# Kernel optimization log

Measured on AMD Instinct MI355X. Metric: run time of the kernel, lower is better.

Reference implementation:

```python
import jax, jax.numpy as jnp
import numpy as np

B, H, E, V = 128, 1024, 1024, 40000
L, S, A = 256, 10, 10
L_S, L_A = 1.0, 1.0  # s_copy_lambda / a_copy_lambda
NEG = -1e24


def setup_inputs():
    key = jax.random.key(0)
    ks = jax.random.split(key, 32)
    n = lambda i, shape: jax.random.normal(ks[i], shape, dtype=jnp.float32)
    p = lambda i, shape: jax.random.normal(ks[i], shape, dtype=jnp.float32) * 0.02
    rnn_in = 3 * E + H  # embed + history ctx (H) + state ctx (E) + action ctx (E)
    return {
        "inp": n(0, (B, 1, E)),
        "hidden": n(1, (1, B, H)),
        "hs_vectors": n(2, (B, L, H)),
        "state_gumbel_prob": jax.random.uniform(ks[3], (B, S, V), dtype=jnp.float32),
        "state_gumbel_embed": n(4, (B, S, E)),
        "action_gumbel_prob": jax.random.uniform(ks[5], (B, A, V), dtype=jnp.float32),
        "action_gumbel_embed": n(6, (B, A, E)),
        "history_lens": jax.random.randint(ks[7], (B,), 1, L + 1),
        "history_word_indices": jax.random.randint(ks[8], (B, L), 0, V),
        # history word mlp-attention
        "Wq_hist": p(9, (H, H)), "bq_hist": jnp.zeros((H,), jnp.float32),
        "Wm_hist": p(10, (H, H)), "v_hist": p(11, (H,)),
        # init_s_attn / init_a_attn (query H, memory E)
        "Wq_s": p(12, (H, H)), "bq_s": jnp.zeros((H,), jnp.float32),
        "Wm_s": p(13, (E, H)), "v_s": p(14, (H,)),
        "Wq_a": p(15, (H, H)), "bq_a": jnp.zeros((H,), jnp.float32),
        "Wm_a": p(16, (E, H)), "v_a": p(17, (H,)),
        # sparse_copy_attn (memory E+1)
        "Wq_sc": p(18, (H, H)), "bq_sc": jnp.zeros((H,), jnp.float32),
        "Wm_sc": p(19, (E + 1, H)), "v_sc": p(20, (H,)),
        # GRU (torch layout: [3H, in], gate order r,z,n)
        "W_ih": p(21, (3 * H, rnn_in)), "W_hh": p(22, (3 * H, H)),
        "b_ih": jnp.zeros((3 * H,), jnp.float32), "b_hh": jnp.zeros((3 * H,), jnp.float32),
        # output projection
        "W_out": p(23, (H, V)), "b_out": jnp.zeros((V,), jnp.float32),
    }


def _mlp_scores(q, mem, Wq, bq, Wm, v):
    # q: [B,1,H], mem: [B,L,M] -> additive-attention logits [B,1,L]
    t = jnp.tanh((q @ Wq + bq) + (mem @ Wm))  # [B,L,H]
    return (t @ v)[:, None, :]


def reference(inp, hidden, hs_vectors, state_gumbel_prob, state_gumbel_embed,
              action_gumbel_prob, action_gumbel_embed, history_lens,
              history_word_indices, Wq_hist, bq_hist, Wm_hist, v_hist,
              Wq_s, bq_s, Wm_s, v_s, Wq_a, bq_a, Wm_a, v_a,
              Wq_sc, bq_sc, Wm_sc, v_sc, W_ih, W_hh, b_ih, b_hh, W_out, b_out):
    q0 = jnp.transpose(hidden, (1, 0, 2))  # [B,1,H]
    # --- history word attention (masked mlp attention) ---
    hist_scores = _mlp_scores(q0, hs_vectors, Wq_hist, bq_hist, Wm_hist, v_hist)
    valid = jnp.arange(L)[None, None, :] < history_lens[:, None, None]
    hist_scores = jnp.where(valid, hist_scores, NEG)
    c_his = jax.nn.softmax(hist_scores, axis=-1) @ hs_vectors  # [B,1,H]
    # --- init_consult over state / action gumbel embeddings ---
    sw = jax.nn.softmax(_mlp_scores(q0, state_gumbel_embed, Wq_s, bq_s, Wm_s, v_s), axis=-1)
    c_state = sw @ state_gumbel_embed  # [B,1,E]
    aw = jax.nn.softmax(_mlp_scores(q0, action_gumbel_embed, Wq_a, bq_a, Wm_a, v_a), axis=-1)
    c_action = aw @ action_gumbel_embed  # [B,1,E]
    x = jnp.concatenate([inp, c_his, c_state, c_action], axis=-1)[:, 0, :]  # [B,3E+H]
    # --- single-step GRU cell (torch semantics, gate order r,z,n) ---
    h0 = hidden[0]
    gi = x @ W_ih.T + b_ih
    gh = h0 @ W_hh.T + b_hh
    ir, iz, inn = jnp.split(gi, 3, axis=-1)
    hr, hz, hn = jnp.split(gh, 3, axis=-1)
    r = jax.nn.sigmoid(ir + hr)
    z = jax.nn.sigmoid(iz + hz)
    nact = jnp.tanh(inn + r * hn)
    h_new = (1.0 - z) * nact + z * h0  # [B,H]
    # --- vocab logits + copy logits, joint softmax ---
    gene_logits = h_new @ W_out + b_out  # [B,V]
    cq = h_new[:, None, :]
    hs_logits = jnp.einsum('bqh,blh->bql', cq, hs_vectors)[:, 0, :]  # dot attn, [B,L]
    s_tag = jnp.zeros((B, S, 1), jnp.float32)
    a_tag = jnp.ones((B, A, 1), jnp.float32)
    st_logits = _mlp_scores(cq, jnp.concatenate([state_gumbel_embed, s_tag], -1), Wq_sc, bq_sc, Wm_sc, v_sc)[:, 0, :]
    ac_logits = _mlp_scores(cq, jnp.concatenate([action_gumbel_embed, a_tag], -1), Wq_sc, bq_sc, Wm_sc, v_sc)[:, 0, :]
    all_logits = jnp.concatenate([gene_logits, hs_logits, st_logits, ac_logits], axis=-1)
    wp = jax.nn.softmax(all_logits, axis=-1)  # [B, V+L+S+A]
    gene_p = wp[:, :V]
    hs_w = wp[:, V:V + L]
    st_w = wp[:, V + L:V + L + S]
    ac_w = wp[:, V + L + S:]
    # --- copy-distribution mixing ---
    scp = jnp.einsum('bs,bsv->bv', st_w, state_gumbel_prob)
    acp = jnp.einsum('ba,bav->bv', ac_w, action_gumbel_prob)
    gene_p = gene_p + L_S * scp + L_A * acp
    copy_p = jnp.zeros((B, V), jnp.float32).at[jnp.arange(B)[:, None], history_word_indices].add(hs_w)
    out = jnp.log(gene_p + copy_p)[:, None, :]  # [B,1,V]
    return out, h_new[None]
```

## Files before the change

kernel.cpp:

```cpp
#include <hip/hip_runtime.h>
#include <stdint.h>

typedef __attribute__((ext_vector_type(4))) float f32x4;
typedef __attribute__((ext_vector_type(2))) unsigned int u32x2;
typedef __attribute__((ext_vector_type(4))) unsigned int u32x4;
typedef __attribute__((ext_vector_type(8))) short bf16x8;

#define BV (128*40000)

__device__ __forceinline__ unsigned rne_bf16(float f) {
    unsigned x = __float_as_uint(f);
    return ((x + 0x7FFFu + ((x >> 16) & 1u)) >> 16) & 0xFFFFu;
}
__device__ __forceinline__ unsigned pack2(float a, float b) {
    return rne_bf16(a) | (rne_bf16(b) << 16);
}
__device__ __forceinline__ float bf2f(unsigned u) {
    return __uint_as_float((u & 0xFFFFu) << 16);
}
__device__ __forceinline__ float sigm(float x) { return 1.0f / (1.0f + expf(-x)); }
__device__ __forceinline__ float ftanh(float x) {
    float e = __expf(2.0f * x);
    return 1.0f - 2.0f / (e + 1.0f);
}

__device__ __forceinline__ void gload16(const void* g, void* l) {
    __builtin_amdgcn_global_load_lds(
        (const __attribute__((address_space(1))) unsigned*)g,
        (__attribute__((address_space(3))) unsigned*)l, 16, 0, 0);
}

struct BigArgs {
    const unsigned short *hs, *WmhT, *se, *ae, *WmsT, *WmaT, *WmscT;
    const float *qh_h, *bq_h, *v_h;
    const float *qh_s, *bq_s, *v_s;
    const float *qh_a, *bq_a, *v_a;
    float *hsc, *stsc, *acsc;
    unsigned short *mseh, *maeh;
};

__global__ __launch_bounds__(512, 1) void k_big(
    BigArgs a, int* __restrict__ ctr, const int* __restrict__ prefix,
    const int* __restrict__ ntp) {
    __shared__ unsigned short As[2][16384];
    __shared__ unsigned short Bs[2][16384];
    __shared__ int sTile;
    __shared__ int rows_tab[256];

    const int nTiles = ntp[0], Mp = ntp[1];
    const int t = threadIdx.x, lane = t & 63, wv = t >> 6;
    const int l16 = lane & 15, lq = lane >> 4;
    const int wm = wv >> 2, wn = wv & 3;
    const int srowL = t >> 3;
    const int gccA = ((t & 7) ^ (srowL & 7)) << 3;
    const int swz = l16 & 7;
    const int c0 = ((lq ^ swz) << 3);
    const int A0 = (wm << 13) + (l16 << 6);
    const int B0 = ((wn >> 1) << 13) + ((((wn & 1) << 6) + l16) << 6);

#define STQA(ktt, d, q) gload16(gAr[q] + (ktt) * 64, &As[d][((q) << 12) + (wv << 9)])
#define STQB(ktt, d, q) gload16(gB + ((size_t)(q) << 16) + (ktt) * 64, &Bs[d][((q) << 12) + (wv << 9)])

    for (;;) {
        __syncthreads();
        if (t == 0) sTile = atomicAdd(ctr, 1);
        __syncthreads();
        const int wg = sTile;
        if (wg >= nTiles) return;

        const unsigned short *Abase, *Bt;
        const float *rb = nullptr, *cb = nullptr, *vv = nullptr;
        float* out = nullptr;
        unsigned short* outh = nullptr;
        int m0, n0, vrows, cls;
        if (wg < 40) {
            cls = 0;
            int op = wg / 20, r = wg - op * 20;
            int mt = r >> 2, nt2 = r & 3;
            if (op == 0) { Abase = a.se; Bt = a.WmsT; rb = a.qh_s; cb = a.bq_s; vv = a.v_s; out = a.stsc; }
            else         { Abase = a.ae; Bt = a.WmaT; rb = a.qh_a; cb = a.bq_a; vv = a.v_a; out = a.acsc; }
            m0 = mt << 8; n0 = nt2 << 8; vrows = 256;
        } else if (wg < 80) {
            cls = 1;
            int r = wg - 40;
            int op = r / 20; r -= op * 20;
            int mt = r >> 2, nt2 = r & 3;
            Abase = op ? a.ae : a.se; Bt = a.WmscT;
            outh = op ? a.maeh : a.mseh;
            m0 = mt << 8; n0 = nt2 << 8; vrows = 256;
        } else {
            cls = 2;
            int h = wg - 80;
            int m = h >> 2, n = h & 3;
            Abase = a.hs; Bt = a.WmhT; rb = a.qh_h; cb = a.bq_h; vv = a.v_h; out = a.hsc;
            m0 = m << 8; n0 = n << 8;
            vrows = Mp - m0; if (vrows > 256) vrows = 256;
        }

        if (t < 256) {
            int rid;
            if (cls != 2) {
                rid = m0 + t;
            } else {
                int g = m0 + t;
                if (g < Mp) {
                    int lo = 0, hi = 128;
                    while (hi - lo > 1) {
                        int mid = (lo + hi) >> 1;
                        if (prefix[mid] <= g) lo = mid; else hi = mid;
                    }
                    rid = (lo << 8) + (g - prefix[lo]);
                } else {
                    rid = 0;
                }
            }
            rows_tab[t] = rid;
        }
        __syncthreads();

        const unsigned short* gAr[4];
#pragma unroll
        for (int q = 0; q < 4; ++q)
            gAr[q] = Abase + ((size_t)rows_tab[srowL + (q << 6)] << 10) + gccA;
        const unsigned short* gB = Bt + (size_t)(n0 + srowL) * 1024 + gccA;

        f32x4 acc[8][4];
#pragma unroll
        for (int i = 0; i < 8; ++i)
#pragma unroll
            for (int j = 0; j < 4; ++j) acc[i][j] = (f32x4){0.f, 0.f, 0.f, 0.f};

        STQA(0, 0, 0); STQA(0, 0, 2);
        STQB(0, 0, 0); STQB(0, 0, 1); STQB(0, 0, 2); STQB(0, 0, 3);
        STQA(0, 0, 1); STQA(0, 0, 3);
        __builtin_amdgcn_sched_barrier(0);
        asm volatile("s_waitcnt vmcnt(2)" ::: "memory");
        __builtin_amdgcn_s_barrier();
        __builtin_amdgcn_sched_barrier(0);

        for (int kt = 0; kt < 16; ++kt) {
            const int cur = kt & 1, dn = cur ^ 1, kn = kt + 1;
            const bool pre = kt < 15;
            const unsigned short* ab = As[cur];
            const unsigned short* bb = Bs[cur];
            bf16x8 bk0[4], bk1[4], af[4];
            if (pre) { STQA(kn, dn, 0); STQA(kn, dn, 2); }
#pragma unroll
            for (int nf = 0; nf < 4; ++nf) bk0[nf] = *(const bf16x8*)(bb + B0 + (nf << 10) + c0);
#pragma unroll
            for (int mf = 0; mf < 4; ++mf) af[mf] = *(const bf16x8*)(ab + A0 + (mf << 10) + c0);
            __builtin_amdgcn_s_setprio(1);
#pragma unroll
            for (int mf = 0; mf < 4; ++mf)
#pragma unroll
                for (int nf = 0; nf < 4; ++nf)
                    acc[mf][nf] = __builtin_amdgcn_mfma_f32_16x16x32_bf16(af[mf], bk0[nf], acc[mf][nf], 0, 0, 0);
            __builtin_amdgcn_s_setprio(0);
            if (pre) { STQB(kn, dn, 0); STQB(kn, dn, 1); }
#pragma unroll
            for (int nf = 0; nf < 4; ++nf) bk1[nf] = *(const bf16x8*)(bb + B0 + (nf << 10) + (c0 ^ 32));
#pragma unroll
            for (int mf = 0; mf < 4; ++mf) af[mf] = *(const bf16x8*)(ab + A0 + (mf << 10) + (c0 ^ 32));
            __builtin_amdgcn_s_setprio(1);
#pragma unroll
            for (int mf = 0; mf < 4; ++mf)
#pragma unroll
                for (int nf = 0; nf < 4; ++nf)
                    acc[mf][nf] = __builtin_amdgcn_mfma_f32_16x16x32_bf16(af[mf], bk1[nf], acc[mf][nf], 0, 0, 0);
            __builtin_amdgcn_s_setprio(0);
            if (pre) { STQB(kn, dn, 2); STQB(kn, dn, 3); }
            __builtin_amdgcn_sched_barrier(0);
            if (pre) asm volatile("s_waitcnt vmcnt(6)" ::: "memory");
            else     asm volatile("s_waitcnt vmcnt(0)" ::: "memory");
            __builtin_amdgcn_s_barrier();
            __builtin_amdgcn_sched_barrier(0);
#pragma unroll
            for (int mf = 0; mf < 4; ++mf) af[mf] = *(const bf16x8*)(ab + A0 + ((4 + mf) << 10) + c0);
            __builtin_amdgcn_s_setprio(1);
#pragma unroll
            for (int mf = 0; mf < 4; ++mf)
#pragma unroll
                for (int nf = 0; nf < 4; ++nf)
                    acc[4 + mf][nf] = __builtin_amdgcn_mfma_f32_16x16x32_bf16(af[mf], bk0[nf], acc[4 + mf][nf], 0, 0, 0);
            __builtin_amdgcn_s_setprio(0);
            if (pre) { STQA(kn, dn, 1); STQA(kn, dn, 3); }
#pragma unroll
            for (int mf = 0; mf < 4; ++mf) af[mf] = *(const bf16x8*)(ab + A0 + ((4 + mf) << 10) + (c0 ^ 32));
            __builtin_amdgcn_s_setprio(1);
#pragma unroll
            for (int mf = 0; mf < 4; ++mf)
#pragma unroll
                for (int nf = 0; nf < 4; ++nf)
                    acc[4 + mf][nf] = __builtin_amdgcn_mfma_f32_16x16x32_bf16(af[mf], bk1[nf], acc[4 + mf][nf], 0, 0, 0);
            __builtin_amdgcn_s_setprio(0);
            __builtin_amdgcn_sched_barrier(0);
            if (pre) asm volatile("s_waitcnt vmcnt(2)" ::: "memory");
            else     asm volatile("s_waitcnt vmcnt(0)" ::: "memory");
            __builtin_amdgcn_s_barrier();
            __builtin_amdgcn_sched_barrier(0);
        }

        if (cls == 1) {
            int gcs4[4];
#pragma unroll
            for (int nf = 0; nf < 4; ++nf) gcs4[nf] = n0 + (wn << 6) + (nf << 4) + l16;
#pragma unroll
            for (int mf = 0; mf < 8; ++mf) {
#pragma unroll
                for (int r = 0; r < 4; ++r) {
                    int grow = m0 + (wm << 7) + (mf << 4) + (lq << 2) + r;
#pragma unroll
                    for (int nf = 0; nf < 4; ++nf)
                        outh[(size_t)grow * 1024 + gcs4[nf]] = (unsigned short)rne_bf16(acc[mf][nf][r]);
                }
            }
        } else {
            float cbv[4], vvv[4];
            int gcs[4];
#pragma unroll
            for (int nf = 0; nf < 4; ++nf) {
                int gc = n0 + (wn << 6) + (nf << 4) + l16;
                gcs[nf] = gc; cbv[nf] = cb[gc]; vvv[nf] = vv[gc];
            }
#pragma unroll
            for (int mf = 0; mf < 8; ++mf) {
                int rloc = (wm << 7) + (mf << 4);
                if (rloc < vrows) {
#pragma unroll
                    for (int r = 0; r < 4; ++r) {
                        int lrow = rloc + (lq << 2) + r;
                        if (lrow >= vrows) continue;
                        int gr = m0 + lrow;
                        int bidx = (cls == 2) ? (rows_tab[lrow] >> 8) : (gr / 10);
                        const float* rbp = rb + ((size_t)bidx << 10);
                        float s = 0.f;
#pragma unroll
                        for (int nf = 0; nf < 4; ++nf) {
                            float x = acc[mf][nf][r] + rbp[gcs[nf]] + cbv[nf];
                            s += ftanh(x) * vvv[nf];
                        }
#pragma unroll
                        for (int m2 = 1; m2 < 16; m2 <<= 1) s += __shfl_xor(s, m2, 64);
                        if (l16 == 0) atomicAdd(&out[gr], s);
                    }
                }
            }
        }
    }
#undef STQA
#undef STQB
}

template<int EPI>
__device__ __forceinline__ void mgemm(
    const unsigned short* __restrict__ A, const unsigned short* __restrict__ Bt,
    float* __restrict__ out,
    int m0, int n0, int kb, int ke, int ldk, int ldc)
{
    __shared__ unsigned short As[2][4096];
    __shared__ unsigned short Bs[2][4096];
    const int t = threadIdx.x, lane = t & 63, wv = t >> 6;
    const int l16 = lane & 15, lq = lane >> 4;
    const int wm = wv >> 1, wn = wv & 1;

    const int srow = lane >> 2, scol = (lane & 3) << 3;
    const unsigned short* gA0 = A + (size_t)(m0 + (wv << 4) + srow) * ldk + kb + scol;
    const unsigned short* gA1 = gA0 + (size_t)64 * ldk;
    const unsigned short* gB0 = Bt + (size_t)(n0 + (wv << 4) + srow) * ldk + kb + scol;
    const unsigned short* gB1 = gB0 + (size_t)64 * ldk;
    unsigned short* lA0 = &As[0][wv << 9];
    unsigned short* lA1 = &As[0][(wv + 4) << 9];
    unsigned short* lB0 = &Bs[0][wv << 9];
    unsigned short* lB1 = &Bs[0][(wv + 4) << 9];

    f32x4 acc[4][4];
#pragma unroll
    for (int i = 0; i < 4; ++i)
#pragma unroll
        for (int j = 0; j < 4; ++j) acc[i][j] = (f32x4){0.f, 0.f, 0.f, 0.f};

    const int NS = (ke - kb) >> 5;
    gload16(gA0, lA0); gload16(gA1, lA1);
    gload16(gB0, lB0); gload16(gB1, lB1);

    for (int s = 0; s < NS; ++s) {
        __syncthreads();
        if (s + 1 < NS) {
            const int nb = (s + 1) & 1, ko = (s + 1) << 5;
            gload16(gA0 + ko, lA0 + (nb << 12)); gload16(gA1 + ko, lA1 + (nb << 12));
            gload16(gB0 + ko, lB0 + (nb << 12)); gload16(gB1 + ko, lB1 + (nb << 12));
        }
        const unsigned short* ab = As[s & 1];
        const unsigned short* bb = Bs[s & 1];
        bf16x8 af[4], bfv[4];
#pragma unroll
        for (int i = 0; i < 4; ++i)
            af[i] = *(const bf16x8*)(ab + (((wm << 6) + (i << 4) + l16) << 5) + (lq << 3));
#pragma unroll
        for (int i = 0; i < 4; ++i)
            bfv[i] = *(const bf16x8*)(bb + (((wn << 6) + (i << 4) + l16) << 5) + (lq << 3));
#pragma unroll
        for (int mf = 0; mf < 4; ++mf)
#pragma unroll
            for (int nf = 0; nf < 4; ++nf)
                acc[mf][nf] = __builtin_amdgcn_mfma_f32_16x16x32_bf16(af[mf], bfv[nf], acc[mf][nf], 0, 0, 0);
    }

#pragma unroll
    for (int mf = 0; mf < 4; ++mf) {
        int gr0 = m0 + (wm << 6) + (mf << 4) + (lq << 2);
#pragma unroll
        for (int nf = 0; nf < 4; ++nf) {
            int gc = n0 + (wn << 6) + (nf << 4) + l16;
#pragma unroll
            for (int r = 0; r < 4; ++r)
                atomicAdd(&out[(size_t)(gr0 + r) * ldc + gc], acc[mf][nf][r]);
        }
    }
}

__device__ __forceinline__ void gene_body(
    const unsigned short* __restrict__ hnb, const float* __restrict__ Wout,
    const float* __restrict__ b_out, float* __restrict__ out, int n0)
{
    __shared__ unsigned short As[2][4096];
    __shared__ unsigned short Bs[2][4096];
    const int t = threadIdx.x, lane = t & 63, wv = t >> 6;
    const int l16 = lane & 15, lq = lane >> 4;
    const int wm = wv >> 1, wn = wv & 1;

    const int srow = lane >> 2, scol = (lane & 3) << 3;
    const unsigned short* gA0 = hnb + (size_t)((wv << 4) + srow) * 1024 + scol;
    const unsigned short* gA1 = gA0 + (size_t)64 * 1024;
    unsigned short* lA0 = &As[0][wv << 9];
    unsigned short* lA1 = &As[0][(wv + 4) << 9];

    const int bn = t & 127, kh = t >> 7;
    const bool ok = (n0 + bn) < 40000;
    const float* gB = Wout + (size_t)(kh * 16) * 40000 + (n0 + bn);

    f32x4 acc[4][4];
#pragma unroll
    for (int i = 0; i < 4; ++i)
#pragma unroll
        for (int j = 0; j < 4; ++j) acc[i][j] = (f32x4){0.f, 0.f, 0.f, 0.f};

    auto stageB = [&](int buf, int ko) {
        const float* src = gB + (size_t)ko * 40000;
        float f[16];
#pragma unroll
        for (int j = 0; j < 16; ++j) f[j] = ok ? src[(size_t)j * 40000] : 0.0f;
        u32x4* d = (u32x4*)&Bs[buf][bn * 32 + kh * 16];
        d[0] = (u32x4){pack2(f[0],f[1]), pack2(f[2],f[3]), pack2(f[4],f[5]), pack2(f[6],f[7])};
        d[1] = (u32x4){pack2(f[8],f[9]), pack2(f[10],f[11]), pack2(f[12],f[13]), pack2(f[14],f[15])};
    };

    gload16(gA0, lA0); gload16(gA1, lA1); stageB(0, 0);
    for (int s = 0; s < 32; ++s) {
        __syncthreads();
        if (s + 1 < 32) {
            const int nb = (s + 1) & 1, ko = (s + 1) << 5;
            gload16(gA0 + ko, lA0 + (nb << 12)); gload16(gA1 + ko, lA1 + (nb << 12));
            stageB(nb, ko);
        }
        const unsigned short* ab = As[s & 1];
        const unsigned short* bb = Bs[s & 1];
        bf16x8 af[4], bfv[4];
#pragma unroll
        for (int i = 0; i < 4; ++i)
            af[i] = *(const bf16x8*)(ab + (((wm << 6) + (i << 4) + l16) << 5) + (lq << 3));
#pragma unroll
        for (int i = 0; i < 4; ++i)
            bfv[i] = *(const bf16x8*)(bb + (((wn << 6) + (i << 4) + l16) << 5) + (lq << 3));
#pragma unroll
        for (int mf = 0; mf < 4; ++mf)
#pragma unroll
            for (int nf = 0; nf < 4; ++nf)
                acc[mf][nf] = __builtin_amdgcn_mfma_f32_16x16x32_bf16(af[mf], bfv[nf], acc[mf][nf], 0, 0, 0);
    }
#pragma unroll
    for (int mf = 0; mf < 4; ++mf) {
        int gr0 = (wm << 6) + (mf << 4) + (lq << 2);
#pragma unroll
        for (int nf = 0; nf < 4; ++nf) {
            int gc = n0 + (wn << 6) + (nf << 4) + l16;
            if (gc < 40000) {
                float bo = b_out[gc];
#pragma unroll
                for (int r = 0; r < 4; ++r)
                    out[(size_t)(gr0 + r) * 40000 + gc] = acc[mf][nf][r] + bo;
            }
        }
    }
}

__global__ __launch_bounds__(256) void k_qh4(
    const unsigned short* q0, const unsigned short* W0, const unsigned short* W1,
    const unsigned short* W2, float* o0, float* o1, float* o2) {
    const unsigned short* W = W0; float* o = o0;
    if (blockIdx.z == 1) { W = W1; o = o1; }
    if (blockIdx.z == 2) { W = W2; o = o2; }
    int kb = blockIdx.y << 8;
    mgemm<2>(q0, W, o, 0, blockIdx.x * 128, kb, kb + 256, 1024, 1024);
}

__global__ __launch_bounds__(256) void k_gigh2(
    const unsigned short* xb, const unsigned short* q0,
    const unsigned short* Wih, const unsigned short* Whh, float* gi, float* gh) {
    if (blockIdx.z == 0) {
        int kb = blockIdx.y << 9;
        mgemm<2>(xb, Wih, gi, 0, blockIdx.x * 128, kb, kb + 512, 4096, 3072);
    } else {
        if (blockIdx.y >= 2) return;
        int kb = blockIdx.y << 9;
        mgemm<2>(q0, Whh, gh, 0, blockIdx.x * 128, kb, kb + 512, 1024, 3072);
    }
}

__global__ __launch_bounds__(256) void k_gene(
    const unsigned short* hnb, const float* Wout, const float* b_out, float* out) {
    gene_body(hnb, Wout, b_out, out, (int)blockIdx.x << 7);
}

struct PrepArgs {
    const float* cs[6]; unsigned short* cd[6]; int pre[7];
    const float* ts[8]; unsigned short* td[8];
    const int* lens; int* prefix; int* nt;
};
__global__ __launch_bounds__(256) void k_prep(PrepArgs a) {
    int bid = blockIdx.x, t = threadIdx.x;
    if (bid < 2048) {
        __shared__ float tile[64][65];
        int z = bid >> 8, rem = bid & 255, y = rem >> 4, x = rem & 15;
        const float* in = a.ts[z];
        unsigned short* ot = a.td[z];
        int k0 = y << 6, n0 = x << 6;
        int tr = t >> 6, tc = t & 63;
#pragma unroll
        for (int i = 0; i < 16; ++i) {
            int r = (i << 2) + tr;
            tile[r][tc] = in[(size_t)(k0 + r) * 1024 + n0 + tc];
        }
        __syncthreads();
#pragma unroll
        for (int i = 0; i < 16; ++i) {
            int r = (i << 2) + tr;
            ot[(size_t)(n0 + r) * 1024 + k0 + tc] = (unsigned short)rne_bf16(tile[tc][r]);
        }
    } else if (bid == 2048) {
        __shared__ int sc[128];
        if (t < 128) sc[t] = a.lens[t];
        __syncthreads();
        for (int off = 1; off < 128; off <<= 1) {
            int x = (t >= off && t < 128) ? sc[t - off] : 0;
            __syncthreads();
            if (t < 128) sc[t] += x;
            __syncthreads();
        }
        if (t == 0) a.prefix[0] = 0;
        if (t < 128) a.prefix[t + 1] = sc[t];
        if (t == 127) {
            int Mp = sc[127];
            a.nt[0] = 80 + (((Mp + 255) >> 8) << 2);
            a.nt[1] = Mp;
        }
    } else {
        int total = a.pre[6];
        for (int i = (bid - 2049) * 256 + t; i < total; i += 2048 * 256) {
            int seg = 0;
            while (i >= a.pre[seg + 1]) ++seg;
            int loc = i - a.pre[seg];
            const f32x4* s4 = (const f32x4*)a.cs[seg] + (size_t)loc * 2;
            f32x4 q0 = s4[0], q1 = s4[1];
            ((u32x4*)a.cd[seg])[loc] =
                (u32x4){pack2(q0[0],q0[1]), pack2(q0[2],q0[3]), pack2(q1[0],q1[1]), pack2(q1[2],q1[3])};
        }
    }
}

__device__ __forceinline__ void softmax10(const float* src, float* dst) {
    float m = src[0];
    for (int i = 1; i < 10; ++i) m = fmaxf(m, src[i]);
    float z = 0.f, e[10];
    for (int i = 0; i < 10; ++i) { e[i] = expf(src[i] - m); z += e[i]; }
    float iz = 1.0f / z;
    for (int i = 0; i < 10; ++i) dst[i] = e[i] * iz;
}

__global__ __launch_bounds__(256) void k_ctx(
    const float* __restrict__ scores, const int* __restrict__ lens,
    const int* __restrict__ prefix,
    const unsigned short* __restrict__ hs,
    const float* __restrict__ inp, const float* __restrict__ st_sc, const float* __restrict__ ac_sc,
    const unsigned short* __restrict__ se, const unsigned short* __restrict__ ae,
    unsigned short* __restrict__ xb) {
    int b = blockIdx.x, t = threadIdx.x;
    __shared__ float w[256];
    __shared__ float red[256];
    __shared__ float sw[10], aw[10];
    int len = lens[b];
    int base = prefix[b];
    bool valid = t < len;
    float s = valid ? scores[base + t] : -3.0e38f;
    red[t] = s;
    __syncthreads();
    for (int st = 128; st > 0; st >>= 1) { if (t < st) red[t] = fmaxf(red[t], red[t + st]); __syncthreads(); }
    float m = red[0];
    __syncthreads();
    float e = valid ? expf(s - m) : 0.0f;
    red[t] = e;
    __syncthreads();
    for (int st = 128; st > 0; st >>= 1) { if (t < st) red[t] += red[t + st]; __syncthreads(); }
    float Z = red[0];
    __syncthreads();
    w[t] = e / Z;
    if (t == 0) softmax10(st_sc + b * 10, sw);
    if (t == 64) softmax10(ac_sc + b * 10, aw);
    f32x4 iv = ((const f32x4*)(inp + (size_t)b * 1024))[t];
    *((u32x2*)(xb + (size_t)b * 4096) + t) = (u32x2){pack2(iv[0], iv[1]), pack2(iv[2], iv[3])};
    __syncthreads();
    float a0 = 0.f, a1 = 0.f, a2 = 0.f, a3 = 0.f;
    for (int l = 0; l < 256; ++l) {
        float wl = w[l];
        if (wl == 0.0f) continue;
        u32x2 u = *((const u32x2*)(hs + ((size_t)b * 256 + l) * 1024) + t);
        a0 += wl * bf2f(u[0]); a1 += wl * bf2f(u[0] >> 16);
        a2 += wl * bf2f(u[1]); a3 += wl * bf2f(u[1] >> 16);
    }
    *((u32x2*)(xb + (size_t)b * 4096 + 1024) + t) = (u32x2){pack2(a0, a1), pack2(a2, a3)};
    float cs0=0,cs1=0,cs2=0,cs3=0, ca0=0,ca1=0,ca2=0,ca3=0;
#pragma unroll
    for (int q = 0; q < 10; ++q) {
        u32x2 us = *((const u32x2*)(se + ((size_t)b * 10 + q) * 1024) + t);
        u32x2 ua = *((const u32x2*)(ae + ((size_t)b * 10 + q) * 1024) + t);
        float ws = sw[q], wa = aw[q];
        cs0 += ws * bf2f(us[0]); cs1 += ws * bf2f(us[0] >> 16);
        cs2 += ws * bf2f(us[1]); cs3 += ws * bf2f(us[1] >> 16);
        ca0 += wa * bf2f(ua[0]); ca1 += wa * bf2f(ua[0] >> 16);
        ca2 += wa * bf2f(ua[1]); ca3 += wa * bf2f(ua[1] >> 16);
    }
    *((u32x2*)(xb + (size_t)b * 4096 + 2048) + t) = (u32x2){pack2(cs0, cs1), pack2(cs2, cs3)};
    *((u32x2*)(xb + (size_t)b * 4096 + 3072) + t) = (u32x2){pack2(ca0, ca1), pack2(ca2, ca3)};
}

__global__ __launch_bounds__(1024) void k_gruhsl(
    const float* __restrict__ gi, const float* __restrict__ gh,
    const float* __restrict__ b_ih, const float* __restrict__ b_hh,
    const float* __restrict__ h0, float* __restrict__ hnew,
    unsigned short* __restrict__ hnb,
    const unsigned short* __restrict__ hs, float* __restrict__ hsl,
    const unsigned short* __restrict__ WqscT, float* __restrict__ qsc) {
    int b = blockIdx.x, y = blockIdx.y, j = threadIdx.x;
    size_t i = (size_t)b * 1024 + j;
    const float* gib = gi + (size_t)b * 3072;
    const float* ghb = gh + (size_t)b * 3072;
    float r = sigm(gib[j] + b_ih[j] + ghb[j] + b_hh[j]);
    float z = sigm(gib[1024 + j] + b_ih[1024 + j] + ghb[1024 + j] + b_hh[1024 + j]);
    float hn = ghb[2048 + j] + b_hh[2048 + j];
    float n = tanhf(gib[2048 + j] + b_ih[2048 + j] + r * hn);
    float h = (1.0f - z) * n + z * h0[i];
    if (y == 0) {
        hnew[i] = h;
        hnb[i] = (unsigned short)rne_bf16(h);
    }
    __shared__ float hsm[1024];
    hsm[j] = h;
    __syncthreads();
    if (y == 0) {
        float acn = 0.f;
        const u32x4* wr = (const u32x4*)(WqscT + ((size_t)j << 10));
#pragma unroll 4
        for (int k8 = 0; k8 < 128; ++k8) {
            u32x4 u = wr[k8];
            const float* hp = hsm + (k8 << 3);
            acn += hp[0]*bf2f(u[0]) + hp[1]*bf2f(u[0]>>16)
                 + hp[2]*bf2f(u[1]) + hp[3]*bf2f(u[1]>>16)
                 + hp[4]*bf2f(u[2]) + hp[5]*bf2f(u[2]>>16)
                 + hp[6]*bf2f(u[3]) + hp[7]*bf2f(u[3]>>16);
        }
        qsc[(size_t)b * 1024 + j] = acn;
    }
    int wave = j >> 6, lane = j & 63;
    float hr[16];
#pragma unroll
    for (int k = 0; k < 16; ++k) hr[k] = hsm[lane * 16 + k];
    for (int l = (y << 7) + wave; l < (y << 7) + 128; l += 16) {
        const u32x4* row = (const u32x4*)(hs + ((size_t)b * 256 + l) * 1024);
        u32x4 u0 = row[lane * 2], u1 = row[lane * 2 + 1];
        float s = hr[0]*bf2f(u0[0]) + hr[1]*bf2f(u0[0]>>16) + hr[2]*bf2f(u0[1]) + hr[3]*bf2f(u0[1]>>16)
                + hr[4]*bf2f(u0[2]) + hr[5]*bf2f(u0[2]>>16) + hr[6]*bf2f(u0[3]) + hr[7]*bf2f(u0[3]>>16)
                + hr[8]*bf2f(u1[0]) + hr[9]*bf2f(u1[0]>>16) + hr[10]*bf2f(u1[1]) + hr[11]*bf2f(u1[1]>>16)
                + hr[12]*bf2f(u1[2]) + hr[13]*bf2f(u1[2]>>16) + hr[14]*bf2f(u1[3]) + hr[15]*bf2f(u1[3]>>16);
#pragma unroll
        for (int msk = 1; msk < 64; msk <<= 1) s += __shfl_xor(s, msk, 64);
        if (lane == 0) hsl[b * 256 + l] = s;
    }
}

__global__ __launch_bounds__(256) void k_smsc(
    const float* __restrict__ gene, const float* __restrict__ hsl,
    const unsigned short* __restrict__ mseh, const unsigned short* __restrict__ maeh,
    const float* __restrict__ qsc, const float* __restrict__ bq_sc,
    const float* __restrict__ v_sc, const float* __restrict__ tagrow,
    const int* __restrict__ hwi, float* __restrict__ stlg, float* __restrict__ aclg,
    float* __restrict__ mbuf, float* __restrict__ zbuf, float* __restrict__ copyp) {
    int b = blockIdx.x, t = threadIdx.x;
    __shared__ float red[256];
    __shared__ float sst[10], sac[10];
    const float* qb = qsc + (size_t)b * 1024;
    for (int s = 0; s < 10; ++s) {
        float ps = 0.f, pa = 0.f;
        const unsigned short* ms = mseh + ((size_t)b * 10 + s) * 1024;
        const unsigned short* ma = maeh + ((size_t)b * 10 + s) * 1024;
#pragma unroll
        for (int k = 0; k < 4; ++k) {
            int c = t + (k << 8);
            float qv = qb[c] + bq_sc[c];
            float vc = v_sc[c];
            ps += ftanh(bf2f(ms[c]) + qv) * vc;
            pa += ftanh(bf2f(ma[c]) + qv + tagrow[c]) * vc;
        }
#pragma unroll
        for (int msk = 1; msk < 64; msk <<= 1) { ps += __shfl_xor(ps, msk, 64); pa += __shfl_xor(pa, msk, 64); }
        if ((t & 63) == 0) { red[t >> 6] = ps; red[4 + (t >> 6)] = pa; }
        __syncthreads();
        if (t == 0) {
            float vs = red[0] + red[1] + red[2] + red[3];
            float va = red[4] + red[5] + red[6] + red[7];
            sst[s] = vs; sac[s] = va;
            stlg[b * 10 + s] = vs; aclg[b * 10 + s] = va;
        }
        __syncthreads();
    }
    const f32x4* g4 = (const f32x4*)(gene + (size_t)b * 40000);
    float mx = -3.0e38f;
    for (int i = t; i < 10000; i += 256) {
        f32x4 q = g4[i];
        mx = fmaxf(mx, fmaxf(fmaxf(q[0], q[1]), fmaxf(q[2], q[3])));
    }
    float hv = hsl[b * 256 + t];
    mx = fmaxf(mx, hv);
    if (t < 10) mx = fmaxf(mx, fmaxf(sst[t], sac[t]));
    red[t] = mx; __syncthreads();
    for (int s = 128; s > 0; s >>= 1) { if (t < s) red[t] = fmaxf(red[t], red[t + s]); __syncthreads(); }
    float m = red[0];
    __syncthreads();
    float sum = 0.f;
    for (int i = t; i < 10000; i += 256) {
        f32x4 q = g4[i];
        sum += expf(q[0]-m) + expf(q[1]-m) + expf(q[2]-m) + expf(q[3]-m);
    }
    sum += expf(hv - m);
    if (t < 10) sum += expf(sst[t] - m) + expf(sac[t] - m);
    red[t] = sum; __syncthreads();
    for (int s = 128; s > 0; s >>= 1) { if (t < s) red[t] += red[t + s]; __syncthreads(); }
    float Z = red[0];
    if (t == 0) { mbuf[b] = m; zbuf[b] = Z; }
    float wv = expf(hv - m) / Z;
    atomicAdd(copyp + (size_t)b * 40000 + hwi[b * 256 + t], wv);
}

__global__ __launch_bounds__(256) void k_final(
    float* __restrict__ gene_out, const float* __restrict__ copyp,
    const float* __restrict__ sprob, const float* __restrict__ aprob,
    const float* __restrict__ stl, const float* __restrict__ acl,
    const float* __restrict__ mbuf, const float* __restrict__ zbuf) {
    int b = blockIdx.y, t = threadIdx.x;
    __shared__ float sw[10], aw[10];
    float m = mbuf[b], iz = 1.0f / zbuf[b];
    if (t < 10) sw[t] = expf(stl[b * 10 + t] - m) * iz;
    if (t >= 64 && t < 74) aw[t - 64] = expf(acl[b * 10 + (t - 64)] - m) * iz;
    __syncthreads();
    int v4 = blockIdx.x * 256 + t;
    if (v4 < 10000) {
        size_t base = (size_t)b * 10000 + v4;
        f32x4 g = ((const f32x4*)gene_out)[base];
        f32x4 c = ((const f32x4*)copyp)[base];
        f32x4 acc;
#pragma unroll
        for (int j = 0; j < 4; ++j) acc[j] = expf(g[j] - m) * iz + c[j];
#pragma unroll
        for (int s = 0; s < 10; ++s) {
            f32x4 pv = ((const f32x4*)sprob)[((size_t)b * 10 + s) * 10000 + v4];
            f32x4 av = ((const f32x4*)aprob)[((size_t)b * 10 + s) * 10000 + v4];
            float ws = sw[s], wa = aw[s];
#pragma unroll
            for (int j = 0; j < 4; ++j) acc[j] += ws * pv[j] + wa * av[j];
        }
        f32x4 r;
#pragma unroll
        for (int j = 0; j < 4; ++j) r[j] = logf(acc[j]);
        ((f32x4*)gene_out)[base] = r;
    }
}

#define OFF_QH_H  0
#define OFF_QH_S  131072
#define OFF_QH_A  262144
#define OFF_QSC   393216
#define OFF_GI    524288
#define OFF_GH    917504
#define OFF_HSC   1310720
#define OFF_STSC  1343488
#define OFF_ACSC  1344768
#define OFF_STLG  1346048
#define OFF_ACLG  1347328
#define OFF_CTR   1348608
#define OFF_PFX   1348736
#define OFF_NT    1348904
#define ZERO_FLOATS 1348936
#define OFF_HSL   1348992
#define OFF_M     1381760
#define OFF_Z     1381888
#define OFF_COPY  1382016
#define FLOAT_TOTAL 6502016
#define SO_HS     0
#define SO_SE     33554432
#define SO_AE     34865152
#define SO_Q0     36175872
#define SO_X      36306944
#define SO_HNB    36831232
#define SO_WQHT   36962304
#define SO_WQST   38010880
#define SO_WQAT   39059456
#define SO_WQSCT  40108032
#define SO_WMHT   41156608
#define SO_WMST   42205184
#define SO_WMAT   43253760
#define SO_WMSCT  44302336
#define SO_WIH    45350912
#define SO_WHH    57933824
#define SO_MSE    61079552
#define SO_MAE    62390272

extern "C" void kernel_launch(void* const* d_in, const int* in_sizes, int n_in,
                              void* d_out, int out_size, void* d_ws, size_t ws_size,
                              hipStream_t stream) {
    const float* inp     = (const float*)d_in[0];
    const float* hidden  = (const float*)d_in[1];
    const float* hs      = (const float*)d_in[2];
    const float* sprob   = (const float*)d_in[3];
    const float* se      = (const float*)d_in[4];
    const float* aprob   = (const float*)d_in[5];
    const float* ae      = (const float*)d_in[6];
    const int*   lens    = (const int*)d_in[7];
    const int*   hwi     = (const int*)d_in[8];
    const float* Wq_hist = (const float*)d_in[9];
    const float* bq_hist = (const float*)d_in[10];
    const float* Wm_hist = (const float*)d_in[11];
    const float* v_hist  = (const float*)d_in[12];
    const float* Wq_s    = (const float*)d_in[13];
    const float* bq_s    = (const float*)d_in[14];
    const float* Wm_s    = (const float*)d_in[15];
    const float* v_s     = (const float*)d_in[16];
    const float* Wq_a    = (const float*)d_in[17];
    const float* bq_a    = (const float*)d_in[18];
    const float* Wm_a    = (const float*)d_in[19];
    const float* v_a     = (const float*)d_in[20];
    const float* Wq_sc   = (const float*)d_in[21];
    const float* bq_sc   = (const float*)d_in[22];
    const float* Wm_sc   = (const float*)d_in[23];
    const float* v_sc    = (const float*)d_in[24];
    const float* W_ih    = (const float*)d_in[25];
    const float* W_hh    = (const float*)d_in[26];
    const float* b_ih    = (const float*)d_in[27];
    const float* b_hh    = (const float*)d_in[28];
    const float* W_out   = (const float*)d_in[29];
    const float* b_out   = (const float*)d_in[30];

    float* out  = (float*)d_out;
    float* w    = (float*)d_ws;
    float* hnew = out + BV;
    unsigned short* sb = (unsigned short*)(w + FLOAT_TOTAL);

    float* qh_h = w + OFF_QH_H;  float* qh_s = w + OFF_QH_S;  float* qh_a = w + OFF_QH_A;
    float* qsc  = w + OFF_QSC;   float* gi   = w + OFF_GI;    float* gh   = w + OFF_GH;
    float* hsc  = w + OFF_HSC;   float* stsc = w + OFF_STSC;  float* acsc = w + OFF_ACSC;
    float* stlg = w + OFF_STLG;  float* aclg = w + OFF_ACLG;
    float* hsl  = w + OFF_HSL;   float* mbuf = w + OFF_M;     float* zbuf = w + OFF_Z;
    float* copyp = w + OFF_COPY;
    int*   ctr  = (int*)(w + OFF_CTR);
    int*   pfx  = (int*)(w + OFF_PFX);
    int*   ntb  = (int*)(w + OFF_NT);

    unsigned short* hs_bf = sb + SO_HS;   unsigned short* se_bf = sb + SO_SE;
    unsigned short* ae_bf = sb + SO_AE;   unsigned short* q0_bf = sb + SO_Q0;
    unsigned short* x_bf  = sb + SO_X;    unsigned short* hnb   = sb + SO_HNB;
    unsigned short* WqhT  = sb + SO_WQHT; unsigned short* WqsT  = sb + SO_WQST;
    unsigned short* WqaT  = sb + SO_WQAT; unsigned short* WqscT = sb + SO_WQSCT;
    unsigned short* WmhT  = sb + SO_WMHT; unsigned short* WmsT  = sb + SO_WMST;
    unsigned short* WmaT  = sb + SO_WMAT; unsigned short* WmscT = sb + SO_WMSCT;
    unsigned short* WihB  = sb + SO_WIH;  unsigned short* WhhB  = sb + SO_WHH;
    unsigned short* mseh  = sb + SO_MSE;  unsigned short* maeh  = sb + SO_MAE;

    dim3 blk(256);

    hipMemsetAsync(w, 0, (size_t)ZERO_FLOATS * 4, stream);
    hipMemsetAsync(copyp, 0, (size_t)BV * 4, stream);

    PrepArgs pa;
    pa.cs[0]=hs; pa.cs[1]=se; pa.cs[2]=ae; pa.cs[3]=hidden; pa.cs[4]=W_ih; pa.cs[5]=W_hh;
    pa.cd[0]=hs_bf; pa.cd[1]=se_bf; pa.cd[2]=ae_bf; pa.cd[3]=q0_bf; pa.cd[4]=WihB; pa.cd[5]=WhhB;
    pa.pre[0]=0; pa.pre[1]=4194304; pa.pre[2]=4358144; pa.pre[3]=4521984;
    pa.pre[4]=4538368; pa.pre[5]=6111232; pa.pre[6]=6504448;
    pa.ts[0]=Wq_hist; pa.ts[1]=Wq_s; pa.ts[2]=Wq_a; pa.ts[3]=Wq_sc;
    pa.ts[4]=Wm_hist; pa.ts[5]=Wm_s; pa.ts[6]=Wm_a; pa.ts[7]=Wm_sc;
    pa.td[0]=WqhT; pa.td[1]=WqsT; pa.td[2]=WqaT; pa.td[3]=WqscT;
    pa.td[4]=WmhT; pa.td[5]=WmsT; pa.td[6]=WmaT; pa.td[7]=WmscT;
    pa.lens = lens; pa.prefix = pfx; pa.nt = ntb;
    k_prep<<<dim3(4097), blk, 0, stream>>>(pa);

    k_qh4<<<dim3(8, 4, 3), blk, 0, stream>>>(q0_bf, WqhT, WqsT, WqaT, qh_h, qh_s, qh_a);

    BigArgs ba;
    ba.hs = hs_bf; ba.WmhT = WmhT; ba.se = se_bf; ba.ae = ae_bf;
    ba.WmsT = WmsT; ba.WmaT = WmaT; ba.WmscT = WmscT;
    ba.qh_h = qh_h; ba.bq_h = bq_hist; ba.v_h = v_hist;
    ba.qh_s = qh_s; ba.bq_s = bq_s; ba.v_s = v_s;
    ba.qh_a = qh_a; ba.bq_a = bq_a; ba.v_a = v_a;
    ba.hsc = hsc; ba.stsc = stsc; ba.acsc = acsc;
    ba.mseh = mseh; ba.maeh = maeh;
    k_big<<<dim3(256), dim3(512), 0, stream>>>(ba, ctr, pfx, ntb);

    k_ctx<<<dim3(128), blk, 0, stream>>>(hsc, lens, pfx, hs_bf, inp, stsc, acsc, se_bf, ae_bf, x_bf);
    k_gigh2<<<dim3(24, 8, 2), blk, 0, stream>>>(x_bf, q0_bf, WihB, WhhB, gi, gh);
    k_gruhsl<<<dim3(128, 2), dim3(1024), 0, stream>>>(gi, gh, b_ih, b_hh, hidden, hnew, hnb,
                                                      hs_bf, hsl, WqscT, qsc);
    k_gene<<<dim3(313), blk, 0, stream>>>(hnb, W_out, b_out, out);
    k_smsc<<<dim3(128), blk, 0, stream>>>(out, hsl, mseh, maeh, qsc, bq_sc, v_sc,
                                          Wm_sc + (size_t)1024 * 1024, hwi, stlg, aclg,
                                          mbuf, zbuf, copyp);
    k_final<<<dim3(40, 128), blk, 0, stream>>>(out, copyp, sprob, aprob, stlg, aclg, mbuf, zbuf);

    (void)in_sizes; (void)n_in; (void)out_size; (void)ws_size;
}
```

Before: 580.8 us.

## Precompute copy-probability mixing alongside gene GEMM and split qsc across blocks

```diff
diff --git a/kernel.cpp b/kernel.cpp
--- a/kernel.cpp
+++ b/kernel.cpp
@@ -251,8 +251,7 @@
 #undef STQB
 }
 
-template<int EPI>
-__device__ __forceinline__ void mgemm(
+__device__ __forceinline__ void mgemm2(
     const unsigned short* __restrict__ A, const unsigned short* __restrict__ Bt,
     float* __restrict__ out,
     int m0, int n0, int kb, int ke, int ldk, int ldc)
@@ -401,7 +400,7 @@
     if (blockIdx.z == 1) { W = W1; o = o1; }
     if (blockIdx.z == 2) { W = W2; o = o2; }
     int kb = blockIdx.y << 8;
-    mgemm<2>(q0, W, o, 0, blockIdx.x * 128, kb, kb + 256, 1024, 1024);
+    mgemm2(q0, W, o, 0, blockIdx.x * 128, kb, kb + 256, 1024, 1024);
 }
 
 __global__ __launch_bounds__(256) void k_gigh2(
@@ -409,17 +408,43 @@
     const unsigned short* Wih, const unsigned short* Whh, float* gi, float* gh) {
     if (blockIdx.z == 0) {
         int kb = blockIdx.y << 9;
-        mgemm<2>(xb, Wih, gi, 0, blockIdx.x * 128, kb, kb + 512, 4096, 3072);
+        mgemm2(xb, Wih, gi, 0, blockIdx.x * 128, kb, kb + 512, 4096, 3072);
     } else {
         if (blockIdx.y >= 2) return;
         int kb = blockIdx.y << 9;
-        mgemm<2>(q0, Whh, gh, 0, blockIdx.x * 128, kb, kb + 512, 1024, 3072);
-    }
-}
-
-__global__ __launch_bounds__(256) void k_gene(
-    const unsigned short* hnb, const float* Wout, const float* b_out, float* out) {
-    gene_body(hnb, Wout, b_out, out, (int)blockIdx.x << 7);
+        mgemm2(q0, Whh, gh, 0, blockIdx.x * 128, kb, kb + 512, 1024, 3072);
+    }
+}
+
+__global__ __launch_bounds__(256) void k_geneR(
+    const unsigned short* __restrict__ hnb, const float* __restrict__ Wout,
+    const float* __restrict__ b_out, float* __restrict__ out,
+    const float* __restrict__ sprob, const float* __restrict__ aprob,
+    const float* __restrict__ wtil, float* __restrict__ R) {
+    int id = blockIdx.x;
+    if (id < 313) {
+        gene_body(hnb, Wout, b_out, out, id << 7);
+        return;
+    }
+    int rid = id - 313;
+    int b = rid / 40, ch = rid - b * 40;
+    int t = threadIdx.x;
+    __shared__ float wsb[20];
+    if (t < 20) wsb[t] = wtil[b * 20 + t];
+    __syncthreads();
+    if (t >= 250) return;
+    int v4 = ch * 250 + t;
+    size_t base = (size_t)b * 10000 + v4;
+    f32x4 r = {0.f, 0.f, 0.f, 0.f};
+#pragma unroll
+    for (int s = 0; s < 10; ++s) {
+        f32x4 pv = ((const f32x4*)sprob)[((size_t)b * 10 + s) * 10000 + v4];
+        f32x4 av = ((const f32x4*)aprob)[((size_t)b * 10 + s) * 10000 + v4];
+        float ws = wsb[s], wa = wsb[10 + s];
+#pragma unroll
+        for (int j = 0; j < 4; ++j) r[j] += ws * pv[j] + wa * av[j];
+    }
+    ((f32x4*)R)[base] = r;
 }
 
 struct PrepArgs {
@@ -566,11 +591,12 @@
     __shared__ float hsm[1024];
     hsm[j] = h;
     __syncthreads();
-    if (y == 0) {
+    {
         float acn = 0.f;
         const u32x4* wr = (const u32x4*)(WqscT + ((size_t)j << 10));
+        int st = y << 6;
 #pragma unroll 4
-        for (int k8 = 0; k8 < 128; ++k8) {
+        for (int k8 = st; k8 < st + 64; ++k8) {
             u32x4 u = wr[k8];
             const float* hp = hsm + (k8 << 3);
             acn += hp[0]*bf2f(u[0]) + hp[1]*bf2f(u[0]>>16)
@@ -578,7 +604,7 @@
                  + hp[4]*bf2f(u[2]) + hp[5]*bf2f(u[2]>>16)
                  + hp[6]*bf2f(u[3]) + hp[7]*bf2f(u[3]>>16);
         }
-        qsc[(size_t)b * 1024 + j] = acn;
+        atomicAdd(&qsc[(size_t)b * 1024 + j], acn);
     }
     int wave = j >> 6, lane = j & 63;
     float hr[16];
@@ -597,41 +623,49 @@
     }
 }
 
-__global__ __launch_bounds__(256) void k_smsc(
-    const float* __restrict__ gene, const float* __restrict__ hsl,
+__global__ __launch_bounds__(256) void k_stacep(
     const unsigned short* __restrict__ mseh, const unsigned short* __restrict__ maeh,
     const float* __restrict__ qsc, const float* __restrict__ bq_sc,
     const float* __restrict__ v_sc, const float* __restrict__ tagrow,
-    const int* __restrict__ hwi, float* __restrict__ stlg, float* __restrict__ aclg,
+    float* __restrict__ stlg, float* __restrict__ aclg,
+    float* __restrict__ mtil, float* __restrict__ wtil) {
+    int b = blockIdx.x, t = threadIdx.x, w = t >> 6, lane = t & 63;
+    __shared__ float res[20];
+    const float* qb = qsc + (size_t)b * 1024;
+    for (int r = w; r < 20; r += 4) {
+        bool ac = r >= 10;
+        int s = ac ? r - 10 : r;
+        const unsigned short* mm = (ac ? maeh : mseh) + ((size_t)b * 10 + s) * 1024;
+        float acc = 0.f;
+#pragma unroll
+        for (int j2 = 0; j2 < 16; ++j2) {
+            int c = lane + (j2 << 6);
+            float x = bf2f(mm[c]) + qb[c] + bq_sc[c];
+            if (ac) x += tagrow[c];
+            acc += ftanh(x) * v_sc[c];
+        }
+#pragma unroll
+        for (int m2 = 1; m2 < 64; m2 <<= 1) acc += __shfl_xor(acc, m2, 64);
+        if (lane == 0) res[r] = acc;
+    }
+    __syncthreads();
+    if (t < 10) stlg[b * 10 + t] = res[t];
+    if (t >= 64 && t < 74) aclg[b * 10 + (t - 64)] = res[10 + (t - 64)];
+    if (t == 128) {
+        float mt = res[0];
+        for (int i2 = 1; i2 < 20; ++i2) mt = fmaxf(mt, res[i2]);
+        mtil[b] = mt;
+        for (int i2 = 0; i2 < 20; ++i2) wtil[b * 20 + i2] = expf(res[i2] - mt);
+    }
+}
+
+__global__ __launch_bounds__(256) void k_smsc(
+    const float* __restrict__ gene, const float* __restrict__ hsl,
+    const float* __restrict__ stl, const float* __restrict__ acl,
+    const int* __restrict__ hwi,
     float* __restrict__ mbuf, float* __restrict__ zbuf, float* __restrict__ copyp) {
     int b = blockIdx.x, t = threadIdx.x;
     __shared__ float red[256];
-    __shared__ float sst[10], sac[10];
-    const float* qb = qsc + (size_t)b * 1024;
-    for (int s = 0; s < 10; ++s) {
-        float ps = 0.f, pa = 0.f;
-        const unsigned short* ms = mseh + ((size_t)b * 10 + s) * 1024;
-        const unsigned short* ma = maeh + ((size_t)b * 10 + s) * 1024;
-#pragma unroll
-        for (int k = 0; k < 4; ++k) {
-            int c = t + (k << 8);
-            float qv = qb[c] + bq_sc[c];
-            float vc = v_sc[c];
-            ps += ftanh(bf2f(ms[c]) + qv) * vc;
-            pa += ftanh(bf2f(ma[c]) + qv + tagrow[c]) * vc;
-        }
-#pragma unroll
-        for (int msk = 1; msk < 64; msk <<= 1) { ps += __shfl_xor(ps, msk, 64); pa += __shfl_xor(pa, msk, 64); }
-        if ((t & 63) == 0) { red[t >> 6] = ps; red[4 + (t >> 6)] = pa; }
-        __syncthreads();
-        if (t == 0) {
-            float vs = red[0] + red[1] + red[2] + red[3];
-            float va = red[4] + red[5] + red[6] + red[7];
-            sst[s] = vs; sac[s] = va;
-            stlg[b * 10 + s] = vs; aclg[b * 10 + s] = va;
-        }
-        __syncthreads();
-    }
     const f32x4* g4 = (const f32x4*)(gene + (size_t)b * 40000);
     float mx = -3.0e38f;
     for (int i = t; i < 10000; i += 256) {
@@ -640,7 +674,7 @@
     }
     float hv = hsl[b * 256 + t];
     mx = fmaxf(mx, hv);
-    if (t < 10) mx = fmaxf(mx, fmaxf(sst[t], sac[t]));
+    if (t < 10) mx = fmaxf(mx, fmaxf(stl[b * 10 + t], acl[b * 10 + t]));
     red[t] = mx; __syncthreads();
     for (int s = 128; s > 0; s >>= 1) { if (t < s) red[t] = fmaxf(red[t], red[t + s]); __syncthreads(); }
     float m = red[0];
@@ -651,7 +685,7 @@
         sum += expf(q[0]-m) + expf(q[1]-m) + expf(q[2]-m) + expf(q[3]-m);
     }
     sum += expf(hv - m);
-    if (t < 10) sum += expf(sst[t] - m) + expf(sac[t] - m);
+    if (t < 10) sum += expf(stl[b * 10 + t] - m) + expf(acl[b * 10 + t] - m);
     red[t] = sum; __syncthreads();
     for (int s = 128; s > 0; s >>= 1) { if (t < s) red[t] += red[t + s]; __syncthreads(); }
     float Z = red[0];
@@ -662,34 +696,21 @@
 
 __global__ __launch_bounds__(256) void k_final(
     float* __restrict__ gene_out, const float* __restrict__ copyp,
-    const float* __restrict__ sprob, const float* __restrict__ aprob,
-    const float* __restrict__ stl, const float* __restrict__ acl,
-    const float* __restrict__ mbuf, const float* __restrict__ zbuf) {
+    const float* __restrict__ R, const float* __restrict__ mbuf,
+    const float* __restrict__ zbuf, const float* __restrict__ mtil) {
     int b = blockIdx.y, t = threadIdx.x;
-    __shared__ float sw[10], aw[10];
-    float m = mbuf[b], iz = 1.0f / zbuf[b];
-    if (t < 10) sw[t] = expf(stl[b * 10 + t] - m) * iz;
-    if (t >= 64 && t < 74) aw[t - 64] = expf(acl[b * 10 + (t - 64)] - m) * iz;
-    __syncthreads();
     int v4 = blockIdx.x * 256 + t;
     if (v4 < 10000) {
+        float m = mbuf[b], iz = 1.0f / zbuf[b];
+        float sb = expf(mtil[b] - m) * iz;
         size_t base = (size_t)b * 10000 + v4;
         f32x4 g = ((const f32x4*)gene_out)[base];
         f32x4 c = ((const f32x4*)copyp)[base];
-        f32x4 acc;
-#pragma unroll
-        for (int j = 0; j < 4; ++j) acc[j] = expf(g[j] - m) * iz + c[j];
-#pragma unroll
-        for (int s = 0; s < 10; ++s) {
-            f32x4 pv = ((const f32x4*)sprob)[((size_t)b * 10 + s) * 10000 + v4];
-            f32x4 av = ((const f32x4*)aprob)[((size_t)b * 10 + s) * 10000 + v4];
-            float ws = sw[s], wa = aw[s];
-#pragma unroll
-            for (int j = 0; j < 4; ++j) acc[j] += ws * pv[j] + wa * av[j];
-        }
+        f32x4 rr = ((const f32x4*)R)[base];
         f32x4 r;
 #pragma unroll
-        for (int j = 0; j < 4; ++j) r[j] = logf(acc[j]);
+        for (int j = 0; j < 4; ++j)
+            r[j] = logf(expf(g[j] - m) * iz + c[j] + rr[j] * sb);
         ((f32x4*)gene_out)[base] = r;
     }
 }
@@ -713,7 +734,9 @@
 #define OFF_M     1381760
 #define OFF_Z     1381888
 #define OFF_COPY  1382016
-#define FLOAT_TOTAL 6502016
+#define OFF_MTIL  6502016
+#define OFF_WTIL  6502144
+#define FLOAT_TOTAL 6504704
 #define SO_HS     0
 #define SO_SE     33554432
 #define SO_AE     34865152
@@ -779,6 +802,7 @@
     float* stlg = w + OFF_STLG;  float* aclg = w + OFF_ACLG;
     float* hsl  = w + OFF_HSL;   float* mbuf = w + OFF_M;     float* zbuf = w + OFF_Z;
     float* copyp = w + OFF_COPY;
+    float* mtil = w + OFF_MTIL;  float* wtil = w + OFF_WTIL;
     int*   ctr  = (int*)(w + OFF_CTR);
     int*   pfx  = (int*)(w + OFF_PFX);
     int*   ntb  = (int*)(w + OFF_NT);
@@ -792,6 +816,7 @@
     unsigned short* WmaT  = sb + SO_WMAT; unsigned short* WmscT = sb + SO_WMSCT;
     unsigned short* WihB  = sb + SO_WIH;  unsigned short* WhhB  = sb + SO_WHH;
     unsigned short* mseh  = sb + SO_MSE;  unsigned short* maeh  = sb + SO_MAE;
+    float* Rbuf = (float*)(sb + SO_WIH);
 
     dim3 blk(256);
 
@@ -826,11 +851,11 @@
     k_gigh2<<<dim3(24, 8, 2), blk, 0, stream>>>(x_bf, q0_bf, WihB, WhhB, gi, gh);
     k_gruhsl<<<dim3(128, 2), dim3(1024), 0, stream>>>(gi, gh, b_ih, b_hh, hidden, hnew, hnb,
                                                       hs_bf, hsl, WqscT, qsc);
-    k_gene<<<dim3(313), blk, 0, stream>>>(hnb, W_out, b_out, out);
-    k_smsc<<<dim3(128), blk, 0, stream>>>(out, hsl, mseh, maeh, qsc, bq_sc, v_sc,
-                                          Wm_sc + (size_t)1024 * 1024, hwi, stlg, aclg,
-                                          mbuf, zbuf, copyp);
-    k_final<<<dim3(40, 128), blk, 0, stream>>>(out, copyp, sprob, aprob, stlg, aclg, mbuf, zbuf);
+    k_stacep<<<dim3(128), blk, 0, stream>>>(mseh, maeh, qsc, bq_sc, v_sc,
+                                            Wm_sc + (size_t)1024 * 1024, stlg, aclg, mtil, wtil);
+    k_geneR<<<dim3(313 + 5120), blk, 0, stream>>>(hnb, W_out, b_out, out, sprob, aprob, wtil, Rbuf);
+    k_smsc<<<dim3(128), blk, 0, stream>>>(out, hsl, stlg, aclg, hwi, mbuf, zbuf, copyp);
+    k_final<<<dim3(40, 128), blk, 0, stream>>>(out, copyp, Rbuf, mbuf, zbuf, mtil);
 
     (void)in_sizes; (void)n_in; (void)out_size; (void)ws_size;
 }
```

After: 561.6 us. 3.3% less time.
